# Performance work log

Hardware: AMD Instinct MI355X
Metric: run time of the kernel (lower is better)

Reference implementation:

```python
import jax, jax.numpy as jnp
import numpy as np

H = 16        # num attention heads
KV = 4        # num key/value heads (GQA)
HD = 128      # head dim
CAP = 50.0    # attn_logits_soft_cap
SCALE = HD ** -0.5
ROPE_THETA = 10000.0


def rotate_half(x):
    return jnp.concatenate([-x[..., HD // 2:], x[..., :HD // 2]], axis=-1)


def setup_inputs() -> dict:
    key = jax.random.key(0)
    k0, k1, k2, k3, k4 = jax.random.split(key, 5)
    B, S, D = 2, 2048, 2048
    hidden_states = jax.random.normal(k0, (B, S, D), dtype=jnp.float32)
    # real rotary tables (HF apply_rotary_pos_emb convention: emb = cat(freqs, freqs))
    pos = jnp.arange(S, dtype=jnp.float32)
    inv_freq = 1.0 / (ROPE_THETA ** (jnp.arange(0, HD, 2, dtype=jnp.float32) / HD))
    freqs = pos[:, None] * inv_freq[None, :]          # [S, HD/2]
    emb = jnp.concatenate([freqs, freqs], axis=-1)    # [S, HD]
    cos = jnp.broadcast_to(jnp.cos(emb)[None], (B, S, HD)).astype(jnp.float32)
    sin = jnp.broadcast_to(jnp.sin(emb)[None], (B, S, HD)).astype(jnp.float32)
    Wq = 0.02 * jax.random.normal(k1, (H * HD, D), dtype=jnp.float32)
    Wk = 0.02 * jax.random.normal(k2, (KV * HD, D), dtype=jnp.float32)
    Wv = 0.02 * jax.random.normal(k3, (KV * HD, D), dtype=jnp.float32)
    Wo = 0.02 * jax.random.normal(k4, (D, H * HD), dtype=jnp.float32)
    return {"hidden_states": hidden_states, "cos": cos, "sin": sin,
            "Wq": Wq, "Wk": Wk, "Wv": Wv, "Wo": Wo}


def reference(hidden_states, cos, sin, Wq, Wk, Wv, Wo):
    B, S, D = hidden_states.shape
    # QKV projections (HF Linear: y = x @ W.T)
    q = jnp.einsum('bsd,hd->bsh', hidden_states, Wq).reshape(B, S, H, HD).transpose(0, 2, 1, 3)
    k = jnp.einsum('bsd,hd->bsh', hidden_states, Wk).reshape(B, S, KV, HD).transpose(0, 2, 1, 3)
    v = jnp.einsum('bsd,hd->bsh', hidden_states, Wv).reshape(B, S, KV, HD).transpose(0, 2, 1, 3)
    # RoPE
    cosb = cos[:, None, :, :]  # [B,1,S,HD]
    sinb = sin[:, None, :, :]
    q = q * cosb + rotate_half(q) * sinb
    k = k * cosb + rotate_half(k) * sinb
    # GQA: repeat kv heads
    rep = H // KV
    k = jnp.repeat(k, rep, axis=1)  # [B,H,S,HD]
    v = jnp.repeat(v, rep, axis=1)
    # splash attention == causal attention with tanh logits soft cap
    scores = jnp.einsum('bhqd,bhkd->bhqk', q * SCALE, k)
    scores = CAP * jnp.tanh(scores / CAP)
    causal = jnp.tril(jnp.ones((S, S), dtype=bool))
    scores = jnp.where(causal[None, None], scores, jnp.float32(-1e30))
    attn = jax.nn.softmax(scores, axis=-1)
    out = jnp.einsum('bhqk,bhkd->bhqd', attn, v)
    out = out.transpose(0, 2, 1, 3).reshape(B, S, H * HD)
    return jnp.einsum('bsh,dh->bsd', out, Wo)
```

## Files before the change

### kernel.cpp

```cpp
#include <hip/hip_runtime.h>
#include <hip/hip_bf16.h>
#include <stdint.h>

typedef __bf16 bf16x8 __attribute__((ext_vector_type(8)));
typedef float f32x4 __attribute__((ext_vector_type(4)));
typedef float f32x16 __attribute__((ext_vector_type(16)));

#define NB_H 16
#define NB_KV 4
#define NB_HD 128
#define NB_B 2
#define NB_S 2048
#define NB_D 2048
#define NB_M (NB_B*NB_S)
#define NB_NQKV 3072
#define CAPF 50.0f
#define SCALEF 0.08838834764831845f

__device__ __forceinline__ ushort f2bf(float x){
  uint32_t u = __float_as_uint(x);
  u += 0x7fffu + ((u >> 16) & 1u);
  return (ushort)(u >> 16);
}
__device__ __forceinline__ float bf2f(ushort u){
  return __uint_as_float(((uint32_t)u) << 16);
}
__device__ __forceinline__ void gload_lds16(const void* g, void* l){
  __builtin_amdgcn_global_load_lds(
      (const __attribute__((address_space(1))) uint32_t*)g,
      (__attribute__((address_space(3))) uint32_t*)l, 16, 0, 0);
}

__global__ __launch_bounds__(256) void cvt_all(const float* __restrict__ hs,
                                               const float* __restrict__ wq,
                                               const float* __restrict__ wk,
                                               const float* __restrict__ wv,
                                               const float* __restrict__ wo,
                                               ushort* __restrict__ hsb,
                                               ushort* __restrict__ wqkv,
                                               ushort* __restrict__ wob){
  int q = blockIdx.x * blockDim.x + threadIdx.x;
  const float* src; ushort* dst; int i;
  if (q < 2097152)      { src = hs; dst = hsb;            i = q; }
  else if (q < 3145728) { src = wq; dst = wqkv;           i = q - 2097152; }
  else if (q < 3407872) { src = wk; dst = wqkv + 4194304; i = q - 3145728; }
  else if (q < 3670016) { src = wv; dst = wqkv + 5242880; i = q - 3407872; }
  else                  { src = wo; dst = wob;            i = q - 3670016; }
  float4 v = ((const float4*)src)[i];
  ushort4 o;
  o.x = f2bf(v.x); o.y = f2bf(v.y); o.z = f2bf(v.z); o.w = f2bf(v.w);
  ((ushort4*)dst)[i] = o;
}

__global__ __launch_bounds__(256) void gemm_bt(const ushort* __restrict__ A,
                                               const ushort* __restrict__ Bw,
                                               ushort* __restrict__ Cb,
                                               float* __restrict__ Cf,
                                               int M, int N, int K, int nbx){
  int nwg = gridDim.x;
  int cpx = nwg >> 3;
  int wg = blockIdx.x;
  int swz = (wg & 7) * cpx + (wg >> 3);
  int bx = swz % nbx, by = swz / nbx;

  __shared__ ushort As[128 * 32];
  __shared__ ushort Bs[128 * 32];
  int tid = threadIdx.x;
  int w = tid >> 6, l = tid & 63;
  int lr = l & 15, lk = l >> 4;
  int row0 = by * 128, col0 = bx * 128;
  int wm = w >> 1, wn = w & 1;

  f32x4 acc[4][4];
#pragma unroll
  for (int mi = 0; mi < 4; ++mi)
#pragma unroll
    for (int nj = 0; nj < 4; ++nj)
      acc[mi][nj] = f32x4{0.f, 0.f, 0.f, 0.f};

  for (int k0 = 0; k0 < K; k0 += 32) {
#pragma unroll
    for (int c = 0; c < 2; ++c) {
      int off = w * 2048 + c * 1024 + l * 16;
      int r = off >> 6;
      int cb = off & 63;
      gload_lds16(A + (size_t)(row0 + r) * K + k0 + (cb >> 1), (char*)As + off);
      gload_lds16(Bw + (size_t)(col0 + r) * K + k0 + (cb >> 1), (char*)Bs + off);
    }
    __syncthreads();
    bf16x8 af[4], bfr[4];
#pragma unroll
    for (int mi = 0; mi < 4; ++mi)
      af[mi] = *(const bf16x8*)(As + (wm * 64 + mi * 16 + lr) * 32 + lk * 8);
#pragma unroll
    for (int nj = 0; nj < 4; ++nj)
      bfr[nj] = *(const bf16x8*)(Bs + (wn * 64 + nj * 16 + lr) * 32 + lk * 8);
    __builtin_amdgcn_s_setprio(1);
#pragma unroll
    for (int mi = 0; mi < 4; ++mi)
#pragma unroll
      for (int nj = 0; nj < 4; ++nj)
        acc[mi][nj] = __builtin_amdgcn_mfma_f32_16x16x32_bf16(af[mi], bfr[nj], acc[mi][nj], 0, 0, 0);
    __builtin_amdgcn_s_setprio(0);
    __syncthreads();
  }

#pragma unroll
  for (int mi = 0; mi < 4; ++mi)
#pragma unroll
    for (int nj = 0; nj < 4; ++nj)
#pragma unroll
      for (int i = 0; i < 4; ++i) {
        int r = row0 + wm * 64 + mi * 16 + lk * 4 + i;
        int c = col0 + wn * 64 + nj * 16 + lr;
        float v = acc[mi][nj][i];
        if (Cb) Cb[(size_t)r * N + c] = f2bf(v);
        else    Cf[(size_t)r * N + c] = v;
      }
}

__global__ __launch_bounds__(256) void rope_kernel(ushort* __restrict__ qkv,
                                                   const float* __restrict__ cosb,
                                                   const float* __restrict__ sinb){
  int idx = blockIdx.x * blockDim.x + threadIdx.x;
  if (idx >= NB_M * 20 * 64) return;
  int row = idx / 1280;
  int rem = idx - row * 1280;
  int head = rem >> 6;
  int d = rem & 63;
  size_t base = (size_t)row * NB_NQKV + head * 128 + d;
  float a = bf2f(qkv[base]);
  float b = bf2f(qkv[base + 64]);
  float c = cosb[row * 128 + d];
  float s = sinb[row * 128 + d];
  qkv[base]      = f2bf(a * c - b * s);
  qkv[base + 64] = f2bf(b * c + a * s);
}

__global__ __launch_bounds__(256) void vtrans_kernel(const ushort* __restrict__ qkv,
                                                     ushort* __restrict__ vt){
  __shared__ ushort tile[64 * 136];
  int bid = blockIdx.x;
  int s0 = (bid & 31) * 64;
  int kvh = (bid >> 5) & 3;
  int b = bid >> 7;
  int tid = threadIdx.x;
#pragma unroll
  for (int i = 0; i < 4; ++i) {
    int g = tid + i * 256;
    int r = g >> 4, c = g & 15;
    *(uint4*)(tile + r * 136 + c * 8) =
        *(const uint4*)(qkv + (size_t)(b * NB_S + s0 + r) * NB_NQKV + 2560 + kvh * 128 + c * 8);
  }
  __syncthreads();
#pragma unroll
  for (int i = 0; i < 4; ++i) {
    int g = tid + i * 256;
    int dd = g >> 3, c = g & 7;
    union { ushort u[8]; uint4 v; } tmp;
#pragma unroll
    for (int j = 0; j < 8; ++j) tmp.u[j] = tile[(c * 8 + j) * 136 + dd];
    *(uint4*)(vt + ((size_t)(b * NB_KV + kvh) * NB_HD + dd) * NB_S + s0 + c * 8) = tmp.v;
  }
}

__global__ __launch_bounds__(256, 2) void attn_kernel(const ushort* __restrict__ qkv,
                                                      const ushort* __restrict__ vt,
                                                      ushort* __restrict__ obuf){
  __shared__ ushort lds[2][16384];
  const int tid = threadIdx.x;
  const int w = tid >> 6, l = tid & 63;
  const int ql = l & 31, hi = l >> 5;
  const int blk = blockIdx.x;
  const int g = blk & 7;
  const int inner = blk >> 3;
  const int j = inner >> 2;
  const int h_lo = inner & 3;
  const int qt = (j < 8) ? (15 - j) : (j - 8);
  const int b = g >> 2, kvh = g & 3;
  const int h = kvh * 4 + h_lo;
  const int qbase = qt * 128 + w * 32;
  const int q = qbase + ql;
  const int nkt = 2 * (qt + 1);

  size_t kidx[4], vidx[4];
#pragma unroll
  for (int i = 0; i < 4; ++i) {
    int s = i * 256 + tid;
    int kr = s >> 4, kc = s & 15;
    int kg = (kc & 8) | ((kc ^ kr) & 7);
    kidx[i] = (size_t)(b * NB_S + kr) * NB_NQKV + 2048 + kvh * 128 + kg * 8;
    int vr = s >> 3, vc = s & 7;
    int vg = (vc ^ vr) & 7;
    vidx[i] = ((size_t)(b * NB_KV + kvh) * NB_HD + vr) * NB_S + vg * 8;
  }

  bf16x8 qf[8];
  {
    const ushort* qrow = qkv + (size_t)(b * NB_S + q) * NB_NQKV + h * 128 + hi * 8;
#pragma unroll
    for (int dc = 0; dc < 8; ++dc)
      qf[dc] = *(const bf16x8*)(qrow + dc * 16);
  }

  f32x16 acc[4];
#pragma unroll
  for (int dt = 0; dt < 4; ++dt)
#pragma unroll
    for (int r = 0; r < 16; ++r) acc[dt][r] = 0.f;
  float l_run = 0.f;

#pragma unroll
  for (int i = 0; i < 4; ++i)
    gload_lds16(qkv + kidx[i], (char*)lds[0] + (i * 256 + tid) * 16);
#pragma unroll
  for (int i = 0; i < 4; ++i)
    gload_lds16(vt + vidx[i], (char*)lds[0] + 16384 + (i * 256 + tid) * 16);
  __syncthreads();

  const float K1 = SCALEF / CAPF;
  const float KW = SCALEF * 1.4426950408889634f;

  int cur = 0;
  for (int kt = 0; kt < nkt; ++kt) {
    const int s0 = kt * 64;
    if (kt + 1 < nkt) {
      const size_t ks = (size_t)(kt + 1) * 64 * NB_NQKV;
      const int vs = (kt + 1) * 64;
#pragma unroll
      for (int i = 0; i < 4; ++i)
        gload_lds16(qkv + kidx[i] + ks, (char*)lds[cur ^ 1] + (i * 256 + tid) * 16);
#pragma unroll
      for (int i = 0; i < 4; ++i)
        gload_lds16(vt + vidx[i] + vs, (char*)lds[cur ^ 1] + 16384 + (i * 256 + tid) * 16);
    }
    const ushort* Kb = lds[cur];
    const ushort* Vb = lds[cur] + 8192;
    if (s0 <= qbase + 31) {
      f32x16 st[2];
#pragma unroll
      for (int t = 0; t < 2; ++t) {
#pragma unroll
        for (int r = 0; r < 16; ++r) st[t][r] = 0.f;
        const int krow = t * 32 + ql;
        __builtin_amdgcn_s_setprio(1);
#pragma unroll
        for (int dc = 0; dc < 8; ++dc) {
          const int gd = dc * 2 + hi;
          const int g2 = (gd & 8) | ((gd ^ krow) & 7);
          bf16x8 kf = *(const bf16x8*)(Kb + krow * 128 + g2 * 8);
          st[t] = __builtin_amdgcn_mfma_f32_32x32x16_bf16(kf, qf[dc], st[t], 0, 0, 0);
        }
        __builtin_amdgcn_s_setprio(0);
      }
      const bool full = (s0 + 63 <= qbase);
      const int qmb = q - s0 - 4 * hi;
      float p[2][16];
      float rs = 0.f;
#pragma unroll
      for (int t = 0; t < 2; ++t)
#pragma unroll
        for (int r = 0; r < 16; ++r) {
          float s = st[t][r];
          float x = s * K1;
          float x2 = x * x;
          float ww = s * KW;
          float t1 = fmaf(x2, 0.13333334f, -0.33333334f);
          float y = fmaf(ww * x2, t1, ww);
          y = fminf(y, 72.134752f);
          if (!full) {
            const int koff = t * 32 + (r & 3) + 8 * (r >> 2);
            y = (koff <= qmb) ? y : -1e30f;
          }
          float pe = __builtin_amdgcn_exp2f(y);
          p[t][r] = pe;
          rs += pe;
        }
      rs += __shfl_xor(rs, 32);
      l_run += rs;
      union { __bf16 hh16[32]; uint u[16]; } Pk;
#pragma unroll
      for (int t = 0; t < 2; ++t)
#pragma unroll
        for (int r = 0; r < 16; ++r)
          Pk.hh16[t * 16 + r] = (__bf16)p[t][r];
      uint rec[2][2][2];
#pragma unroll
      for (int t = 0; t < 2; ++t)
#pragma unroll
        for (int hh = 0; hh < 2; ++hh)
#pragma unroll
          for (int wb = 0; wb < 2; ++wb) {
            uint send = hi ? Pk.u[t * 8 + 4 * hh + wb] : Pk.u[t * 8 + 4 * hh + 2 + wb];
            rec[t][hh][wb] = __shfl_xor(send, 32);
          }
#pragma unroll
      for (int c = 0; c < 4; ++c) {
        const int t = c >> 1, hh = c & 1;
        union { uint u[4]; bf16x8 v; } pf;
        pf.u[0] = hi ? rec[t][hh][0] : Pk.u[t * 8 + 4 * hh + 0];
        pf.u[1] = hi ? rec[t][hh][1] : Pk.u[t * 8 + 4 * hh + 1];
        pf.u[2] = hi ? Pk.u[t * 8 + 4 * hh + 2] : rec[t][hh][0];
        pf.u[3] = hi ? Pk.u[t * 8 + 4 * hh + 3] : rec[t][hh][1];
        __builtin_amdgcn_s_setprio(1);
#pragma unroll
        for (int dt = 0; dt < 4; ++dt) {
          const int vrow = dt * 32 + ql;
          const int gk = c * 2 + hi;
          const int g2 = (gk ^ vrow) & 7;
          bf16x8 vf = *(const bf16x8*)(Vb + vrow * 64 + g2 * 8);
          acc[dt] = __builtin_amdgcn_mfma_f32_32x32x16_bf16(vf, pf.v, acc[dt], 0, 0, 0);
        }
        __builtin_amdgcn_s_setprio(0);
      }
    }
    __syncthreads();
    cur ^= 1;
  }

  const float inv = __builtin_amdgcn_rcpf(l_run);
  ushort* reg = (ushort*)lds + (size_t)w * 4352;
#pragma unroll
  for (int dt = 0; dt < 4; ++dt)
#pragma unroll
    for (int gg = 0; gg < 4; ++gg) {
      ushort4 o;
      o.x = f2bf(acc[dt][4 * gg + 0] * inv);
      o.y = f2bf(acc[dt][4 * gg + 1] * inv);
      o.z = f2bf(acc[dt][4 * gg + 2] * inv);
      o.w = f2bf(acc[dt][4 * gg + 3] * inv);
      const int d0 = dt * 32 + gg * 8 + hi * 4;
      *(ushort4*)(reg + ql * 136 + d0) = o;
    }
  __syncthreads();
#pragma unroll
  for (int i = 0; i < 8; ++i) {
    const int qr = i * 4 + (l >> 4);
    const int c = l & 15;
    uint4 v = *(const uint4*)(reg + qr * 136 + c * 8);
    *(uint4*)(obuf + (size_t)(b * NB_S + qbase + qr) * NB_D + h * 128 + c * 8) = v;
  }
}

extern "C" void kernel_launch(void* const* d_in, const int* in_sizes, int n_in,
                              void* d_out, int out_size, void* d_ws, size_t ws_size,
                              hipStream_t stream) {
  const float* hs   = (const float*)d_in[0];
  const float* cosb = (const float*)d_in[1];
  const float* sinb = (const float*)d_in[2];
  const float* Wq   = (const float*)d_in[3];
  const float* Wk   = (const float*)d_in[4];
  const float* Wv   = (const float*)d_in[5];
  const float* Wo   = (const float*)d_in[6];
  float* out = (float*)d_out;
  char* ws = (char*)d_ws;

  ushort* hsb  = (ushort*)(ws + 0);
  ushort* wqkv = (ushort*)(ws + 16777216);
  ushort* wob  = (ushort*)(ws + 29360128);
  ushort* qkvb = (ushort*)(ws + 37748736);
  ushort* vtb  = (ushort*)(ws + 62914560);
  ushort* ob   = (ushort*)(ws + 67108864);

  cvt_all<<<18432, 256, 0, stream>>>(hs, Wq, Wk, Wv, Wo, hsb, wqkv, wob);

  gemm_bt<<<768, 256, 0, stream>>>(hsb, wqkv, qkvb, nullptr, NB_M, NB_NQKV, NB_D, 24);
  rope_kernel<<<(NB_M * 20 * 64 + 255) / 256, 256, 0, stream>>>(qkvb, cosb, sinb);
  vtrans_kernel<<<NB_B * NB_KV * (NB_S / 64), 256, 0, stream>>>(qkvb, vtb);

  attn_kernel<<<512, 256, 0, stream>>>(qkvb, vtb, ob);

  gemm_bt<<<512, 256, 0, stream>>>(ob, wob, nullptr, out, NB_M, NB_D, NB_D, 16);
}
```

Baseline: 364.2 us.

## Split attention KV loop across two waves per 32-query tile, drop LDS staging

The attention kernel now runs 2048 blocks of 128 threads, each handling a 32-query tile. The two waves split the key tiles between them by stride, and their partial accumulators and row sums are combined through LDS at the end. K and V fragments are loaded straight from global memory instead of being double-buffered into LDS with async loads. The split-KV scheme gives finer-grained parallelism and better causal load balance. In exchange it loses LDS data reuse across queries, so the same K/V data is read from global/L2 many more times, and the 64-key tiles are no longer shared by four waves.

```diff
diff --git a/kernel.cpp b/kernel.cpp
--- a/kernel.cpp
+++ b/kernel.cpp
@@ -164,36 +164,28 @@
   }
 }
 
-__global__ __launch_bounds__(256, 2) void attn_kernel(const ushort* __restrict__ qkv,
+__global__ __launch_bounds__(128, 4) void attn_kernel(const ushort* __restrict__ qkv,
                                                       const ushort* __restrict__ vt,
                                                       ushort* __restrict__ obuf){
-  __shared__ ushort lds[2][16384];
+  __shared__ float accbuf[4096];
+  __shared__ float lbuf[64];
+  __shared__ ushort trbuf[32 * 140];
   const int tid = threadIdx.x;
   const int w = tid >> 6, l = tid & 63;
   const int ql = l & 31, hi = l >> 5;
   const int blk = blockIdx.x;
   const int g = blk & 7;
   const int inner = blk >> 3;
-  const int j = inner >> 2;
   const int h_lo = inner & 3;
-  const int qt = (j < 8) ? (15 - j) : (j - 8);
+  const int qtile = 63 - (inner >> 2);
   const int b = g >> 2, kvh = g & 3;
   const int h = kvh * 4 + h_lo;
-  const int qbase = qt * 128 + w * 32;
-  const int q = qbase + ql;
-  const int nkt = 2 * (qt + 1);
-
-  size_t kidx[4], vidx[4];
-#pragma unroll
-  for (int i = 0; i < 4; ++i) {
-    int s = i * 256 + tid;
-    int kr = s >> 4, kc = s & 15;
-    int kg = (kc & 8) | ((kc ^ kr) & 7);
-    kidx[i] = (size_t)(b * NB_S + kr) * NB_NQKV + 2048 + kvh * 128 + kg * 8;
-    int vr = s >> 3, vc = s & 7;
-    int vg = (vc ^ vr) & 7;
-    vidx[i] = ((size_t)(b * NB_KV + kvh) * NB_HD + vr) * NB_S + vg * 8;
-  }
+  const int q0 = qtile * 32;
+  const int q = q0 + ql;
+  const int nkt = (q0 + 95) >> 6;
+
+  const ushort* Kg = qkv + (size_t)b * NB_S * NB_NQKV + 2048 + kvh * 128;
+  const ushort* Vg = vt + (size_t)(b * NB_KV + kvh) * NB_HD * NB_S;
 
   bf16x8 qf[8];
   {
@@ -210,135 +202,117 @@
     for (int r = 0; r < 16; ++r) acc[dt][r] = 0.f;
   float l_run = 0.f;
 
-#pragma unroll
-  for (int i = 0; i < 4; ++i)
-    gload_lds16(qkv + kidx[i], (char*)lds[0] + (i * 256 + tid) * 16);
-#pragma unroll
-  for (int i = 0; i < 4; ++i)
-    gload_lds16(vt + vidx[i], (char*)lds[0] + 16384 + (i * 256 + tid) * 16);
-  __syncthreads();
-
   const float K1 = SCALEF / CAPF;
   const float KW = SCALEF * 1.4426950408889634f;
 
-  int cur = 0;
-  for (int kt = 0; kt < nkt; ++kt) {
+  for (int kt = w; kt < nkt; kt += 2) {
     const int s0 = kt * 64;
-    if (kt + 1 < nkt) {
-      const size_t ks = (size_t)(kt + 1) * 64 * NB_NQKV;
-      const int vs = (kt + 1) * 64;
-#pragma unroll
-      for (int i = 0; i < 4; ++i)
-        gload_lds16(qkv + kidx[i] + ks, (char*)lds[cur ^ 1] + (i * 256 + tid) * 16);
-#pragma unroll
-      for (int i = 0; i < 4; ++i)
-        gload_lds16(vt + vidx[i] + vs, (char*)lds[cur ^ 1] + 16384 + (i * 256 + tid) * 16);
+    f32x16 st[2];
+#pragma unroll
+    for (int t = 0; t < 2; ++t) {
+#pragma unroll
+      for (int r = 0; r < 16; ++r) st[t][r] = 0.f;
+      const ushort* krow = Kg + (size_t)(s0 + t * 32 + ql) * NB_NQKV + hi * 8;
+#pragma unroll
+      for (int dc = 0; dc < 8; ++dc) {
+        bf16x8 kf = *(const bf16x8*)(krow + dc * 16);
+        st[t] = __builtin_amdgcn_mfma_f32_32x32x16_bf16(kf, qf[dc], st[t], 0, 0, 0);
+      }
     }
-    const ushort* Kb = lds[cur];
-    const ushort* Vb = lds[cur] + 8192;
-    if (s0 <= qbase + 31) {
-      f32x16 st[2];
-#pragma unroll
-      for (int t = 0; t < 2; ++t) {
-#pragma unroll
-        for (int r = 0; r < 16; ++r) st[t][r] = 0.f;
-        const int krow = t * 32 + ql;
-        __builtin_amdgcn_s_setprio(1);
-#pragma unroll
-        for (int dc = 0; dc < 8; ++dc) {
-          const int gd = dc * 2 + hi;
-          const int g2 = (gd & 8) | ((gd ^ krow) & 7);
-          bf16x8 kf = *(const bf16x8*)(Kb + krow * 128 + g2 * 8);
-          st[t] = __builtin_amdgcn_mfma_f32_32x32x16_bf16(kf, qf[dc], st[t], 0, 0, 0);
+    const bool full = (s0 + 63 <= q0);
+    const int qmb = q - s0 - 4 * hi;
+    float p[2][16];
+    float rs = 0.f;
+#pragma unroll
+    for (int t = 0; t < 2; ++t)
+#pragma unroll
+      for (int r = 0; r < 16; ++r) {
+        float s = st[t][r];
+        float x = s * K1;
+        float x2 = x * x;
+        float ww = s * KW;
+        float t1 = fmaf(x2, 0.13333334f, -0.33333334f);
+        float y = fmaf(ww * x2, t1, ww);
+        y = fminf(y, 72.134752f);
+        if (!full) {
+          const int koff = t * 32 + (r & 3) + 8 * (r >> 2);
+          y = (koff <= qmb) ? y : -1e30f;
         }
-        __builtin_amdgcn_s_setprio(0);
-      }
-      const bool full = (s0 + 63 <= qbase);
-      const int qmb = q - s0 - 4 * hi;
-      float p[2][16];
-      float rs = 0.f;
-#pragma unroll
-      for (int t = 0; t < 2; ++t)
-#pragma unroll
-        for (int r = 0; r < 16; ++r) {
-          float s = st[t][r];
-          float x = s * K1;
-          float x2 = x * x;
-          float ww = s * KW;
-          float t1 = fmaf(x2, 0.13333334f, -0.33333334f);
-          float y = fmaf(ww * x2, t1, ww);
-          y = fminf(y, 72.134752f);
-          if (!full) {
-            const int koff = t * 32 + (r & 3) + 8 * (r >> 2);
-            y = (koff <= qmb) ? y : -1e30f;
-          }
-          float pe = __builtin_amdgcn_exp2f(y);
-          p[t][r] = pe;
-          rs += pe;
+        float pe = __builtin_amdgcn_exp2f(y);
+        p[t][r] = pe;
+        rs += pe;
+      }
+    rs += __shfl_xor(rs, 32);
+    l_run += rs;
+    union { __bf16 hh16[32]; uint u[16]; } Pk;
+#pragma unroll
+    for (int t = 0; t < 2; ++t)
+#pragma unroll
+      for (int r = 0; r < 16; ++r)
+        Pk.hh16[t * 16 + r] = (__bf16)p[t][r];
+    uint rec[2][2][2];
+#pragma unroll
+    for (int t = 0; t < 2; ++t)
+#pragma unroll
+      for (int hh = 0; hh < 2; ++hh)
+#pragma unroll
+        for (int wb = 0; wb < 2; ++wb) {
+          uint send = hi ? Pk.u[t * 8 + 4 * hh + wb] : Pk.u[t * 8 + 4 * hh + 2 + wb];
+          rec[t][hh][wb] = __shfl_xor(send, 32);
         }
-      rs += __shfl_xor(rs, 32);
-      l_run += rs;
-      union { __bf16 hh16[32]; uint u[16]; } Pk;
-#pragma unroll
-      for (int t = 0; t < 2; ++t)
-#pragma unroll
-        for (int r = 0; r < 16; ++r)
-          Pk.hh16[t * 16 + r] = (__bf16)p[t][r];
-      uint rec[2][2][2];
-#pragma unroll
-      for (int t = 0; t < 2; ++t)
-#pragma unroll
-        for (int hh = 0; hh < 2; ++hh)
-#pragma unroll
-          for (int wb = 0; wb < 2; ++wb) {
-            uint send = hi ? Pk.u[t * 8 + 4 * hh + wb] : Pk.u[t * 8 + 4 * hh + 2 + wb];
-            rec[t][hh][wb] = __shfl_xor(send, 32);
-          }
-#pragma unroll
-      for (int c = 0; c < 4; ++c) {
-        const int t = c >> 1, hh = c & 1;
-        union { uint u[4]; bf16x8 v; } pf;
-        pf.u[0] = hi ? rec[t][hh][0] : Pk.u[t * 8 + 4 * hh + 0];
-        pf.u[1] = hi ? rec[t][hh][1] : Pk.u[t * 8 + 4 * hh + 1];
-        pf.u[2] = hi ? Pk.u[t * 8 + 4 * hh + 2] : rec[t][hh][0];
-        pf.u[3] = hi ? Pk.u[t * 8 + 4 * hh + 3] : rec[t][hh][1];
-        __builtin_amdgcn_s_setprio(1);
-#pragma unroll
-        for (int dt = 0; dt < 4; ++dt) {
-          const int vrow = dt * 32 + ql;
-          const int gk = c * 2 + hi;
-          const int g2 = (gk ^ vrow) & 7;
-          bf16x8 vf = *(const bf16x8*)(Vb + vrow * 64 + g2 * 8);
-          acc[dt] = __builtin_amdgcn_mfma_f32_32x32x16_bf16(vf, pf.v, acc[dt], 0, 0, 0);
-        }
-        __builtin_amdgcn_s_setprio(0);
+#pragma unroll
+    for (int c = 0; c < 4; ++c) {
+      const int t = c >> 1, hh = c & 1;
+      union { uint u[4]; bf16x8 v; } pf;
+      pf.u[0] = hi ? rec[t][hh][0] : Pk.u[t * 8 + 4 * hh + 0];
+      pf.u[1] = hi ? rec[t][hh][1] : Pk.u[t * 8 + 4 * hh + 1];
+      pf.u[2] = hi ? Pk.u[t * 8 + 4 * hh + 2] : rec[t][hh][0];
+      pf.u[3] = hi ? Pk.u[t * 8 + 4 * hh + 3] : rec[t][hh][1];
+#pragma unroll
+      for (int dt = 0; dt < 4; ++dt) {
+        bf16x8 vf = *(const bf16x8*)(Vg + (size_t)(dt * 32 + ql) * NB_S + s0 + (c * 2 + hi) * 8);
+        acc[dt] = __builtin_amdgcn_mfma_f32_32x32x16_bf16(vf, pf.v, acc[dt], 0, 0, 0);
       }
     }
-    __syncthreads();
-    cur ^= 1;
-  }
-
-  const float inv = __builtin_amdgcn_rcpf(l_run);
-  ushort* reg = (ushort*)lds + (size_t)w * 4352;
-#pragma unroll
-  for (int dt = 0; dt < 4; ++dt)
-#pragma unroll
-    for (int gg = 0; gg < 4; ++gg) {
-      ushort4 o;
-      o.x = f2bf(acc[dt][4 * gg + 0] * inv);
-      o.y = f2bf(acc[dt][4 * gg + 1] * inv);
-      o.z = f2bf(acc[dt][4 * gg + 2] * inv);
-      o.w = f2bf(acc[dt][4 * gg + 3] * inv);
-      const int d0 = dt * 32 + gg * 8 + hi * 4;
-      *(ushort4*)(reg + ql * 136 + d0) = o;
-    }
+  }
+
+  if (w == 1) {
+#pragma unroll
+    for (int dt = 0; dt < 4; ++dt)
+#pragma unroll
+      for (int r = 0; r < 16; ++r)
+        accbuf[(dt * 16 + r) * 64 + l] = acc[dt][r];
+    lbuf[l] = l_run;
+  }
   __syncthreads();
-#pragma unroll
-  for (int i = 0; i < 8; ++i) {
-    const int qr = i * 4 + (l >> 4);
-    const int c = l & 15;
-    uint4 v = *(const uint4*)(reg + qr * 136 + c * 8);
-    *(uint4*)(obuf + (size_t)(b * NB_S + qbase + qr) * NB_D + h * 128 + c * 8) = v;
+  if (w == 0) {
+#pragma unroll
+    for (int dt = 0; dt < 4; ++dt)
+#pragma unroll
+      for (int r = 0; r < 16; ++r)
+        acc[dt][r] += accbuf[(dt * 16 + r) * 64 + l];
+    l_run += lbuf[l];
+    const float inv = __builtin_amdgcn_rcpf(l_run);
+#pragma unroll
+    for (int dt = 0; dt < 4; ++dt)
+#pragma unroll
+      for (int gg = 0; gg < 4; ++gg) {
+        ushort4 o;
+        o.x = f2bf(acc[dt][4 * gg + 0] * inv);
+        o.y = f2bf(acc[dt][4 * gg + 1] * inv);
+        o.z = f2bf(acc[dt][4 * gg + 2] * inv);
+        o.w = f2bf(acc[dt][4 * gg + 3] * inv);
+        const int d0 = dt * 32 + gg * 8 + hi * 4;
+        *(ushort4*)(trbuf + ql * 140 + d0) = o;
+      }
+  }
+  __syncthreads();
+#pragma unroll
+  for (int i = 0; i < 4; ++i) {
+    const int qr = i * 8 + (tid >> 4);
+    const int c = tid & 15;
+    uint4 v = *(const uint4*)(trbuf + qr * 140 + c * 8);
+    *(uint4*)(obuf + (size_t)(b * NB_S + q0 + qr) * NB_D + h * 128 + c * 8) = v;
   }
 }
 
@@ -368,7 +342,7 @@
   rope_kernel<<<(NB_M * 20 * 64 + 255) / 256, 256, 0, stream>>>(qkvb, cosb, sinb);
   vtrans_kernel<<<NB_B * NB_KV * (NB_S / 64), 256, 0, stream>>>(qkvb, vtb);
 
-  attn_kernel<<<512, 256, 0, stream>>>(qkvb, vtb, ob);
+  attn_kernel<<<2048, 128, 0, stream>>>(qkvb, vtb, ob);
 
   gemm_bt<<<512, 256, 0, stream>>>(ob, wob, nullptr, out, NB_M, NB_D, NB_D, 16);
 }
```

New measurement: 427.2 us. 1.17x slower.
